# Optimization experiments

Hardware: AMD Instinct MI355X
Metric: run time of the kernel (lower is better)

Reference implementation:

```python
import jax, jax.numpy as jnp
import numpy as np

# --- MLA config (DeepSeek-V3 style, scaled) ---
HIDDEN = 4096
N_HEADS = 32
Q_LORA = 1536
KV_LORA = 512
ROPE_D = 64
NOPE_D = 128
V_D = 128
Q_HEAD_D = NOPE_D + ROPE_D  # 192
EPS = 1e-6
SCALING = Q_HEAD_D ** (-0.5)
ROPE_THETA = 10000.0
B, S = 1, 2048


def rms_norm(x, w):
    var = jnp.mean(jnp.square(x.astype(jnp.float32)), axis=-1, keepdims=True)
    return (x * jax.lax.rsqrt(var + EPS)).astype(x.dtype) * w


def rotate_half(x):
    x1, x2 = jnp.split(x, 2, axis=-1)
    return jnp.concatenate([-x2, x1], axis=-1)


def apply_rope(x, cos, sin):
    # x: [B, H, S, ROPE_D]; cos/sin: [B, S, ROPE_D] -> unsqueeze head dim
    c = cos[:, None, :, :]
    s = sin[:, None, :, :]
    return x * c + rotate_half(x) * s


def setup_inputs() -> dict:
    key = jax.random.key(0)
    ks = jax.random.split(key, 8)
    hidden_states = jax.random.normal(ks[0], (B, S, HIDDEN), dtype=jnp.float32)
    # real RoPE tables
    inv_freq = 1.0 / (ROPE_THETA ** (np.arange(0, ROPE_D, 2, dtype=np.float32) / ROPE_D))
    t = np.arange(S, dtype=np.float32)
    freqs = np.outer(t, inv_freq)                      # [S, ROPE_D/2]
    emb = np.concatenate([freqs, freqs], axis=-1)      # [S, ROPE_D]
    cos = jnp.asarray(np.cos(emb))[None].repeat(B, 0)  # [B, S, ROPE_D]
    sin = jnp.asarray(np.sin(emb))[None].repeat(B, 0)
    scale = lambda fan_in: 1.0 / np.sqrt(fan_in)
    w_q_a = jax.random.normal(ks[1], (Q_LORA, HIDDEN), dtype=jnp.float32) * scale(HIDDEN)
    q_a_ln_w = jnp.ones((Q_LORA,), dtype=jnp.float32)
    w_q_b = jax.random.normal(ks[2], (N_HEADS * Q_HEAD_D, Q_LORA), dtype=jnp.float32) * scale(Q_LORA)
    w_kv_a = jax.random.normal(ks[3], (KV_LORA + ROPE_D, HIDDEN), dtype=jnp.float32) * scale(HIDDEN)
    kv_a_ln_w = jnp.ones((KV_LORA,), dtype=jnp.float32)
    w_kv_b = jax.random.normal(ks[4], (N_HEADS * (NOPE_D + V_D), KV_LORA), dtype=jnp.float32) * scale(KV_LORA)
    w_o = jax.random.normal(ks[5], (HIDDEN, N_HEADS * V_D), dtype=jnp.float32) * scale(N_HEADS * V_D)
    return {
        'hidden_states': hidden_states, 'cos': cos, 'sin': sin,
        'w_q_a': w_q_a, 'q_a_ln_w': q_a_ln_w, 'w_q_b': w_q_b,
        'w_kv_a': w_kv_a, 'kv_a_ln_w': kv_a_ln_w, 'w_kv_b': w_kv_b, 'w_o': w_o,
    }


def reference(hidden_states, cos, sin, w_q_a, q_a_ln_w, w_q_b, w_kv_a, kv_a_ln_w, w_kv_b, w_o):
    b, s, _ = hidden_states.shape
    # --- Q path: low-rank down + RMSNorm + up ---
    q_lat = rms_norm(hidden_states @ w_q_a.T, q_a_ln_w)              # [B,S,Q_LORA]
    q = (q_lat @ w_q_b.T).reshape(b, s, N_HEADS, Q_HEAD_D)
    q = q.transpose(0, 2, 1, 3)                                       # [B,H,S,Q_HEAD_D]
    q_nope, q_rot = q[..., :NOPE_D], q[..., NOPE_D:]                  # (note: source names swapped)
    # --- KV path: shared compressed latent + single rotary key ---
    ckv = hidden_states @ w_kv_a.T                                    # [B,S,KV_LORA+ROPE_D]
    k_lat, k_rot = ckv[..., :KV_LORA], ckv[..., KV_LORA:]
    kv = (rms_norm(k_lat, kv_a_ln_w) @ w_kv_b.T).reshape(b, s, N_HEADS, NOPE_D + V_D)
    kv = kv.transpose(0, 2, 1, 3)                                     # [B,H,S,NOPE_D+V_D]
    k_nope, v = kv[..., :NOPE_D], kv[..., NOPE_D:]
    k_rot = k_rot.reshape(b, 1, s, ROPE_D)                            # single rotary key head
    # --- partial RoPE on rotary slices ---
    q_rot = apply_rope(q_rot, cos, sin)
    k_rot = apply_rope(k_rot, cos, sin)
    k_rot = jnp.broadcast_to(k_rot, (b, N_HEADS, s, ROPE_D))
    query = jnp.concatenate([q_rot, q_nope], axis=-1)                 # [B,H,S,192]
    key = jnp.concatenate([k_rot, k_nope], axis=-1)                   # [B,H,S,192]
    # --- eager causal attention ---
    scores = jnp.einsum('bhqd,bhkd->bhqk', query, key) * SCALING
    causal = jnp.tril(jnp.ones((s, s), dtype=bool))
    scores = jnp.where(causal[None, None], scores, jnp.finfo(scores.dtype).min)
    probs = jax.nn.softmax(scores, axis=-1)
    attn = jnp.einsum('bhqk,bhkd->bhqd', probs, v)                    # [B,H,S,V_D]
    attn = attn.transpose(0, 2, 1, 3).reshape(b, s, N_HEADS * V_D)
    return attn @ w_o.T                                               # [B,S,HIDDEN]
```

## Files before the change

kernel.cpp:

```cpp
#include <hip/hip_runtime.h>

typedef unsigned short u16;
typedef u16 u16x4 __attribute__((ext_vector_type(4)));
typedef u16 u16x8 __attribute__((ext_vector_type(8)));
typedef float f32x4 __attribute__((ext_vector_type(4)));
typedef __bf16 bf16x8 __attribute__((ext_vector_type(8)));

#define S_LEN 2048
#define HIDDEN_D 4096
#define NHEADS 32
#define QLORA 1536
#define KVLORA 512
#define ROPED 64
#define NOPED 128
#define VDIM 128
#define QHD 192
#define SCALING_F 0.07216878364870323f

__device__ __forceinline__ u16 f2bf(float x) {
  union { float f; unsigned u; } v; v.f = x;
  unsigned r = v.u + 0x7fffu + ((v.u >> 16) & 1u);
  return (u16)(r >> 16);
}
__device__ __forceinline__ float bf2f(u16 x) {
  union { unsigned u; float f; } v; v.u = ((unsigned)x) << 16; return v.f;
}

__device__ __forceinline__ f32x4 mfma_bf16(u16x8 a, u16x8 b, f32x4 c) {
  return __builtin_amdgcn_mfma_f32_16x16x32_bf16(
      __builtin_bit_cast(bf16x8, a), __builtin_bit_cast(bf16x8, b), c, 0, 0, 0);
}

__global__ __launch_bounds__(256) void cvt_kernel(const float* __restrict__ in,
                                                  u16* __restrict__ out, int n4) {
  int i = blockIdx.x * 256 + threadIdx.x;
  if (i >= n4) return;
  f32x4 v = ((const f32x4*)in)[i];
  u16x4 o;
  o[0] = f2bf(v[0]); o[1] = f2bf(v[1]); o[2] = f2bf(v[2]); o[3] = f2bf(v[3]);
  ((u16x4*)out)[i] = o;
}


#define GEMM_PROLOGUE()                                                        \
  __shared__ u16 sA[2][128 * 64];                                              \
  __shared__ u16 sB[2][128 * 64];                                              \
  const int tid = threadIdx.x;                                                 \
  const int wid = tid >> 6, lane = tid & 63;                                   \
  const int lr = lane & 15, lg = lane >> 4;                                    \
  const int nbn = (N + 127) >> 7;                                              \
  const int bx = blockIdx.x % nbn, by = blockIdx.x / nbn;                      \
  const int bm = by << 7, bn = bx << 7;                                        \
  const int wm = (wid >> 1) << 6, wn = (wid & 1) << 6;                         \
  const int kbase = blockIdx.y * Ks;                                           \
  f32x4 acc[4][4] = {};                                                        \
  u16x8 areg[4], breg[4];                                                      \
  auto loadA = [&](int k0) {                                                   \
    _Pragma("unroll")                                                          \
    for (int i = 0; i < 4; ++i) {                                              \
      int chunk = i * 256 + tid;                                               \
      int row = chunk >> 3, c8 = chunk & 7;                                    \
      int gr = bm + row; if (gr >= M) gr = M - 1;                              \
      areg[i] = *(const u16x8*)(A + (size_t)gr * lda + k0 + (c8 << 3));        \
    }                                                                          \
  };                                                                           \
  auto loadB = [&](int k0) {                                                   \
    _Pragma("unroll")                                                          \
    for (int i = 0; i < 4; ++i) {                                              \
      int chunk = i * 256 + tid;                                               \
      int n = chunk >> 3, c8 = chunk & 7;                                      \
      int gn = bn + n; if (gn >= N) gn = N - 1;                                \
      breg[i] = *(const u16x8*)(B + (size_t)gn * ldb + k0 + (c8 << 3));        \
    }                                                                          \
  };                                                                           \
  auto writeAB = [&](int buf) {                                                \
    _Pragma("unroll")                                                          \
    for (int i = 0; i < 4; ++i) {                                              \
      *(u16x8*)&sA[buf][(i * 256 + tid) * 8] = areg[i];                        \
      *(u16x8*)&sB[buf][(i * 256 + tid) * 8] = breg[i];                        \
    }                                                                          \
  };                                                                           \
  auto compute = [&](int buf) {                                                \
    const u16* pa = sA[buf];                                                   \
    const u16* pb = sB[buf];                                                   \
    _Pragma("unroll")                                                          \
    for (int ks = 0; ks < 2; ++ks) {                                           \
      const int kof = ks * 32 + lg * 8;                                        \
      u16x8 av[4], bv[4];                                                      \
      _Pragma("unroll")                                                        \
      for (int m = 0; m < 4; ++m) av[m] = *(const u16x8*)&pa[(wm + m * 16 + lr) * 64 + kof]; \
      _Pragma("unroll")                                                        \
      for (int n = 0; n < 4; ++n) bv[n] = *(const u16x8*)&pb[(wn + n * 16 + lr) * 64 + kof]; \
      _Pragma("unroll")                                                        \
      for (int m = 0; m < 4; ++m)                                              \
        _Pragma("unroll")                                                      \
        for (int n = 0; n < 4; ++n)                                            \
          acc[m][n] = mfma_bf16(av[m], bv[n], acc[m][n]);                      \
    }                                                                          \
  };                                                                           \
  const int nk = Ks >> 6;                                                      \
  loadA(kbase); loadB(kbase);                                                  \
  writeAB(0);                                                                  \
  __syncthreads();                                                             \
  for (int t = 0; t < nk; ++t) {                                               \
    const int cur = t & 1;                                                     \
    if (t + 1 < nk) { loadA(kbase + ((t + 1) << 6)); loadB(kbase + ((t + 1) << 6)); } \
    compute(cur);                                                              \
    if (t + 1 < nk) { writeAB(cur ^ 1); }                                      \
    __syncthreads();                                                           \
  }

__global__ __launch_bounds__(256, 2) void gemm_ff(
    const u16* __restrict__ A, const u16* __restrict__ B, float* __restrict__ C,
    int M, int N, int Ks, int lda, int ldb, int ldc)
{
  C += (size_t)blockIdx.y * M * ldc;
  GEMM_PROLOGUE()
#pragma unroll
  for (int m = 0; m < 4; ++m) {
    const int row0 = bm + wm + m * 16 + (lg << 2);
#pragma unroll
    for (int n = 0; n < 4; ++n) {
      const int col = bn + wn + n * 16 + lr;
      if (col < N) {
#pragma unroll
        for (int r = 0; r < 4; ++r)
          C[(size_t)(row0 + r) * ldc + col] = acc[m][n][r];
      }
    }
  }
}

__global__ __launch_bounds__(256, 2) void gemm_fb(
    const u16* __restrict__ A, const u16* __restrict__ B, u16* __restrict__ C,
    int M, int N, int Ks, int lda, int ldb, int ldc)
{
  GEMM_PROLOGUE()
#pragma unroll
  for (int m = 0; m < 4; ++m) {
    const int row0 = bm + wm + m * 16 + (lg << 2);
#pragma unroll
    for (int n = 0; n < 4; ++n) {
      const int col = bn + wn + n * 16 + lr;
#pragma unroll
      for (int r = 0; r < 4; ++r)
        C[(size_t)(row0 + r) * ldc + col] = f2bf(acc[m][n][r]);
    }
  }
}

__global__ __launch_bounds__(256, 2) void gemm_kvb(
    const u16* __restrict__ A, const u16* __restrict__ B,
    u16* __restrict__ Knope, u16* __restrict__ Vt,
    int M, int N, int Ks, int lda, int ldb)
{
  GEMM_PROLOGUE()
#pragma unroll
  for (int m = 0; m < 4; ++m) {
    const int row0 = bm + wm + m * 16 + (lg << 2);
#pragma unroll
    for (int n = 0; n < 4; ++n) {
      const int col = bn + wn + n * 16 + lr;
      const int h = col >> 8, c = col & 255;
      if (c < 128) {
#pragma unroll
        for (int r = 0; r < 4; ++r)
          Knope[((size_t)h * 2048 + row0 + r) * 128 + c] = f2bf(acc[m][n][r]);
      } else {
        u16x4 v;
        v[0] = f2bf(acc[m][n][0]); v[1] = f2bf(acc[m][n][1]);
        v[2] = f2bf(acc[m][n][2]); v[3] = f2bf(acc[m][n][3]);
        *(u16x4*)&Vt[((size_t)h * 128 + (c - 128)) * 2048 + row0] = v;
      }
    }
  }
}

__global__ __launch_bounds__(256) void rms_kernel(const float* __restrict__ X,
                                                  const float* __restrict__ w,
                                                  u16* __restrict__ out, int D, int ldx,
                                                  int nparts, size_t pstride) {
  const int row = blockIdx.x;
  const float* x = X + (size_t)row * ldx;
  __shared__ float sb[4];
  float ss = 0.f;
  for (int i = threadIdx.x * 4; i < D; i += 1024) {
    f32x4 v = *(const f32x4*)&x[i];
    for (int pp = 1; pp < nparts; ++pp) {
      f32x4 v2 = *(const f32x4*)&x[pp * pstride + i];
      v[0] += v2[0]; v[1] += v2[1]; v[2] += v2[2]; v[3] += v2[3];
    }
    ss += v[0] * v[0] + v[1] * v[1] + v[2] * v[2] + v[3] * v[3];
  }
#pragma unroll
  for (int off = 32; off >= 1; off >>= 1) ss += __shfl_xor(ss, off, 64);
  if ((threadIdx.x & 63) == 0) sb[threadIdx.x >> 6] = ss;
  __syncthreads();
  const float inv = rsqrtf((sb[0] + sb[1] + sb[2] + sb[3]) / (float)D + 1e-6f);
  u16* o = out + (size_t)row * D;
  for (int i = threadIdx.x * 4; i < D; i += 1024) {
    f32x4 v = *(const f32x4*)&x[i];
    for (int pp = 1; pp < nparts; ++pp) {
      f32x4 v2 = *(const f32x4*)&x[pp * pstride + i];
      v[0] += v2[0]; v[1] += v2[1]; v[2] += v2[2]; v[3] += v2[3];
    }
    f32x4 wv = *(const f32x4*)&w[i];
    u16x4 u;
    u[0] = f2bf(v[0] * inv * wv[0]); u[1] = f2bf(v[1] * inv * wv[1]);
    u[2] = f2bf(v[2] * inv * wv[2]); u[3] = f2bf(v[3] * inv * wv[3]);
    *(u16x4*)&o[i] = u;
  }
}

__global__ __launch_bounds__(256) void ckv_epi_kernel(const float* __restrict__ ckv,
    const float* __restrict__ w, const float* __restrict__ cosp, const float* __restrict__ sinp,
    u16* __restrict__ klatn, u16* __restrict__ krot, int ldx, int nparts, size_t pstride) {
  const int s = blockIdx.x;
  const float* x = ckv + (size_t)s * ldx;
  __shared__ float sb[4];
  const int i2 = threadIdx.x * 2;
  float a = 0.f, b = 0.f;
  for (int pp = 0; pp < nparts; ++pp) {
    a += x[pp * pstride + i2];
    b += x[pp * pstride + i2 + 1];
  }
  float ss = a * a + b * b;
#pragma unroll
  for (int off = 32; off >= 1; off >>= 1) ss += __shfl_xor(ss, off, 64);
  if ((threadIdx.x & 63) == 0) sb[threadIdx.x >> 6] = ss;
  __syncthreads();
  const float inv = rsqrtf((sb[0] + sb[1] + sb[2] + sb[3]) / 512.0f + 1e-6f);
  klatn[(size_t)s * 512 + i2]     = f2bf(a * inv * w[i2]);
  klatn[(size_t)s * 512 + i2 + 1] = f2bf(b * inv * w[i2 + 1]);
  if (threadIdx.x < 64) {
    const int d = threadIdx.x;
    float xr = 0.f, rrabs = 0.f;
    for (int pp = 0; pp < nparts; ++pp) {
      xr += x[pp * pstride + 512 + d];
      rrabs += x[pp * pstride + 512 + ((d < 32) ? (d + 32) : (d - 32))];
    }
    const float rr = (d < 32) ? -rrabs : rrabs;
    krot[(size_t)s * 64 + d] = f2bf(xr * cosp[s * 64 + d] + rr * sinp[s * 64 + d]);
  }
}

__global__ __launch_bounds__(256) void q_epi_kernel(const u16* __restrict__ q_raw,
    const float* __restrict__ cosp, const float* __restrict__ sinp, u16* __restrict__ Qb) {
  const int s = blockIdx.x;
  const u16* x = q_raw + (size_t)s * 6144;
  for (int idx = threadIdx.x; idx < 6144; idx += 256) {
    const int h = idx / 192, d = idx - h * 192;
    float v;
    if (d < 64) {
      const float xr = bf2f(x[h * 192 + 128 + d]);
      const float rr = (d < 32) ? -bf2f(x[h * 192 + 160 + d]) : bf2f(x[h * 192 + 96 + d]);
      v = xr * cosp[s * 64 + d] + rr * sinp[s * 64 + d];
    } else {
      v = bf2f(x[h * 192 + d - 64]);
    }
    Qb[((size_t)h * 2048 + s) * QHD + d] = f2bf(v * SCALING_F);
  }
}

__global__ __launch_bounds__(256, 2) void flash_kernel(
    const u16* __restrict__ Qb, const u16* __restrict__ Krot,
    const u16* __restrict__ Knope, const u16* __restrict__ Vt,
    u16* __restrict__ attnb)
{
  const int h = blockIdx.x & 31, qt = blockIdx.x >> 5;
  const int q0 = qt << 7;
  __shared__ u16 sK[64][QHD];
  __shared__ u16 sV[VDIM][64];
  __shared__ u16 sP[4][32][64];
  const int tid = threadIdx.x;
  const int wid = tid >> 6, lane = tid & 63;
  const int lr = lane & 15, lg = lane >> 4;

  u16x8 qf[2][6];
#pragma unroll
  for (int m = 0; m < 2; ++m) {
    const int row = q0 + wid * 32 + m * 16 + lr;
#pragma unroll
    for (int kk = 0; kk < 6; ++kk)
      qf[m][kk] = *(const u16x8*)&Qb[((size_t)h * 2048 + row) * QHD + kk * 32 + lg * 8];
  }

  f32x4 acc[2][8] = {};
  float mx[2][4], ls[2][4];
#pragma unroll
  for (int m = 0; m < 2; ++m)
#pragma unroll
    for (int r = 0; r < 4; ++r) { mx[m][r] = -1e30f; ls[m][r] = 0.f; }

  const int nkv = q0 + 128;
  u16x8 kreg[6], vreg[4];

  auto loadKV = [&](int kv0) {
#pragma unroll
    for (int i = 0; i < 6; ++i) {
      const int chunk = i * 256 + tid;
      const int row = chunk / 24, cc = chunk % 24;
      const u16* src = (cc < 8)
          ? &Krot[(size_t)(kv0 + row) * 64 + cc * 8]
          : &Knope[((size_t)h * 2048 + kv0 + row) * 128 + (cc - 8) * 8];
      kreg[i] = *(const u16x8*)src;
    }
#pragma unroll
    for (int i = 0; i < 4; ++i) {
      const int chunk = i * 256 + tid;
      const int d = chunk >> 3, c = chunk & 7;
      vreg[i] = *(const u16x8*)&Vt[((size_t)h * VDIM + d) * 2048 + kv0 + c * 8];
    }
  };

  loadKV(0);
  for (int kv0 = 0; kv0 < nkv; kv0 += 64) {
    __syncthreads();
    u16* kbase = &sK[0][0];
#pragma unroll
    for (int i = 0; i < 6; ++i) *(u16x8*)&kbase[(size_t)(i * 256 + tid) * 8] = kreg[i];
    u16* vbase = &sV[0][0];
#pragma unroll
    for (int i = 0; i < 4; ++i) *(u16x8*)&vbase[(size_t)(i * 256 + tid) * 8] = vreg[i];
    __syncthreads();
    if (kv0 + 64 < nkv) loadKV(kv0 + 64);

    f32x4 sc[2][4] = {};
#pragma unroll
    for (int kk = 0; kk < 6; ++kk) {
      u16x8 bfr[4];
#pragma unroll
      for (int n = 0; n < 4; ++n) bfr[n] = *(const u16x8*)&sK[n * 16 + lr][kk * 32 + lg * 8];
#pragma unroll
      for (int m = 0; m < 2; ++m)
#pragma unroll
        for (int n = 0; n < 4; ++n)
          sc[m][n] = mfma_bf16(qf[m][kk], bfr[n], sc[m][n]);
    }

    if (kv0 + 63 > q0 + wid * 32) {
#pragma unroll
      for (int m = 0; m < 2; ++m)
#pragma unroll
        for (int n = 0; n < 4; ++n) {
          const int kv = kv0 + n * 16 + lr;
#pragma unroll
          for (int r = 0; r < 4; ++r) {
            const int rowq = q0 + wid * 32 + m * 16 + lg * 4 + r;
            if (kv > rowq) sc[m][n][r] = -1e30f;
          }
        }
    }

#pragma unroll
    for (int m = 0; m < 2; ++m) {
      float rs[4];
#pragma unroll
      for (int r = 0; r < 4; ++r) {
        float v = fmaxf(fmaxf(sc[m][0][r], sc[m][1][r]), fmaxf(sc[m][2][r], sc[m][3][r]));
#pragma unroll
        for (int off = 1; off < 16; off <<= 1) v = fmaxf(v, __shfl_xor(v, off, 64));
        const float mnew = fmaxf(mx[m][r], v);
        const float alpha = __expf(mx[m][r] - mnew);
        mx[m][r] = mnew;
        ls[m][r] *= alpha;
#pragma unroll
        for (int df = 0; df < 8; ++df) acc[m][df][r] *= alpha;
        rs[r] = 0.f;
      }
#pragma unroll
      for (int n = 0; n < 4; ++n)
#pragma unroll
        for (int r = 0; r < 4; ++r) {
          const float p = __expf(sc[m][n][r] - mx[m][r]);
          rs[r] += p;
          sP[wid][m * 16 + lg * 4 + r][n * 16 + lr] = f2bf(p);
        }
#pragma unroll
      for (int r = 0; r < 4; ++r) {
        float v = rs[r];
#pragma unroll
        for (int off = 1; off < 16; off <<= 1) v += __shfl_xor(v, off, 64);
        ls[m][r] += v;
      }
    }

#pragma unroll
    for (int ks = 0; ks < 2; ++ks) {
      u16x8 pf0 = *(const u16x8*)&sP[wid][lr][ks * 32 + lg * 8];
      u16x8 pf1 = *(const u16x8*)&sP[wid][16 + lr][ks * 32 + lg * 8];
#pragma unroll
      for (int df = 0; df < 8; ++df) {
        u16x8 vf = *(const u16x8*)&sV[df * 16 + lr][ks * 32 + lg * 8];
        acc[0][df] = mfma_bf16(pf0, vf, acc[0][df]);
        acc[1][df] = mfma_bf16(pf1, vf, acc[1][df]);
      }
    }
  }

#pragma unroll
  for (int m = 0; m < 2; ++m)
#pragma unroll
    for (int df = 0; df < 8; ++df) {
      const int col = h * 128 + df * 16 + lr;
#pragma unroll
      for (int r = 0; r < 4; ++r) {
        const int row = q0 + wid * 32 + m * 16 + lg * 4 + r;
        attnb[(size_t)row * 4096 + col] = f2bf(acc[m][df][r] / ls[m][r]);
      }
    }
}

extern "C" void kernel_launch(void* const* d_in, const int* in_sizes, int n_in,
                              void* d_out, int out_size, void* d_ws, size_t ws_size,
                              hipStream_t stream) {
  (void)in_sizes; (void)n_in; (void)out_size; (void)ws_size;
  const float* hidden  = (const float*)d_in[0];
  const float* cosp    = (const float*)d_in[1];
  const float* sinp    = (const float*)d_in[2];
  const float* w_q_a   = (const float*)d_in[3];
  const float* q_a_ln  = (const float*)d_in[4];
  const float* w_q_b   = (const float*)d_in[5];
  const float* w_kv_a  = (const float*)d_in[6];
  const float* kv_a_ln = (const float*)d_in[7];
  const float* w_kv_b  = (const float*)d_in[8];
  const float* w_o     = (const float*)d_in[9];
  float* out = (float*)d_out;

  char* p = (char*)d_ws;
  auto alloc = [&](size_t bytes) { char* r = p; p += (bytes + 255) & ~(size_t)255; return r; };
  u16* Hb      = (u16*)alloc((size_t)S_LEN * HIDDEN_D * 2);
  u16* qlatn   = (u16*)alloc((size_t)S_LEN * QLORA * 2);
  u16* klatn   = (u16*)alloc((size_t)S_LEN * KVLORA * 2);
  u16* krot    = (u16*)alloc((size_t)S_LEN * ROPED * 2);
  u16* Qb      = (u16*)alloc((size_t)NHEADS * S_LEN * QHD * 2);
  u16* Knope   = (u16*)alloc((size_t)NHEADS * S_LEN * NOPED * 2);
  u16* Vt      = (u16*)alloc((size_t)NHEADS * VDIM * S_LEN * 2);
  u16* attnb   = (u16*)alloc((size_t)S_LEN * 4096 * 2);
  u16* WqaKva  = (u16*)alloc((size_t)2112 * HIDDEN_D * 2);
  u16* Wqb     = (u16*)alloc((size_t)6144 * QLORA * 2);
  u16* Wkvb    = (u16*)alloc((size_t)8192 * KVLORA * 2);
  u16* Wo      = (u16*)alloc((size_t)HIDDEN_D * 4096 * 2);
  u16* qraw16  = (u16*)alloc((size_t)S_LEN * 6144 * 2);
  float* qkv_part = (float*)alloc((size_t)2 * S_LEN * 2112 * 4);

  cvt_kernel<<<(S_LEN * HIDDEN_D / 4 + 255) / 256, 256, 0, stream>>>(hidden, Hb, S_LEN * HIDDEN_D / 4);
  cvt_kernel<<<(QLORA * HIDDEN_D / 4 + 255) / 256, 256, 0, stream>>>(w_q_a, WqaKva, QLORA * HIDDEN_D / 4);
  cvt_kernel<<<(576 * HIDDEN_D / 4 + 255) / 256, 256, 0, stream>>>(w_kv_a, WqaKva + (size_t)QLORA * HIDDEN_D, 576 * HIDDEN_D / 4);
  cvt_kernel<<<(6144 * QLORA / 4 + 255) / 256, 256, 0, stream>>>(w_q_b, Wqb, 6144 * QLORA / 4);
  cvt_kernel<<<(8192 * KVLORA / 4 + 255) / 256, 256, 0, stream>>>(w_kv_b, Wkvb, 8192 * KVLORA / 4);
  cvt_kernel<<<(HIDDEN_D * 4096 / 4 + 255) / 256, 256, 0, stream>>>(w_o, Wo, HIDDEN_D * 4096 / 4);

  gemm_ff<<<dim3(16 * 17, 2), 256, 0, stream>>>(Hb, WqaKva, qkv_part, 2048, 2112, 2048, 4096, 4096, 2112);
  rms_kernel<<<2048, 256, 0, stream>>>(qkv_part, q_a_ln, qlatn, 1536, 2112, 2, (size_t)S_LEN * 2112);
  ckv_epi_kernel<<<2048, 256, 0, stream>>>(qkv_part + 1536, kv_a_ln, cosp, sinp, klatn, krot, 2112, 2, (size_t)S_LEN * 2112);
  gemm_fb<<<dim3(16 * 48, 1), 256, 0, stream>>>(qlatn, Wqb, qraw16, 2048, 6144, 1536, 1536, 1536, 6144);
  q_epi_kernel<<<2048, 256, 0, stream>>>(qraw16, cosp, sinp, Qb);
  gemm_kvb<<<dim3(16 * 64, 1), 256, 0, stream>>>(klatn, Wkvb, Knope, Vt, 2048, 8192, 512, 512, 512);
  flash_kernel<<<512, 256, 0, stream>>>(Qb, krot, Knope, Vt, attnb);
  gemm_ff<<<dim3(16 * 32, 1), 256, 0, stream>>>(attnb, Wo, out, 2048, 4096, 4096, 4096, 4096, 4096);
}
```

Before: 598.9 us.

## Fuse q_b RoPE epilogue into GEMM, merge launches, permute Wqb rows

The five weight and activation conversion launches become one multi-range kernel. w_q_b is converted with a per-head row permutation so the rope columns come first. That lets the q_b GEMM apply RoPE and scaling in its epilogue and write Qb directly, removing the bf16 q_raw intermediate and the q_epi pass. The two RMS-norm kernels are merged into one launch, and the q_b and kv_b GEMMs now share a single grid. This trades fewer launches and less memory traffic for more scattered, uncoalesced epilogue stores and extra cos/sin loads per element.

```diff
diff --git a/kernel.cpp b/kernel.cpp
--- a/kernel.cpp
+++ b/kernel.cpp
@@ -31,25 +31,46 @@
       __builtin_bit_cast(bf16x8, a), __builtin_bit_cast(bf16x8, b), c, 0, 0, 0);
 }
 
-__global__ __launch_bounds__(256) void cvt_kernel(const float* __restrict__ in,
-                                                  u16* __restrict__ out, int n4) {
-  int i = blockIdx.x * 256 + threadIdx.x;
-  if (i >= n4) return;
-  f32x4 v = ((const f32x4*)in)[i];
+__global__ __launch_bounds__(256) void cvt_all(
+    const float* __restrict__ hsrc, u16* __restrict__ Hb,
+    const float* __restrict__ wqa, const float* __restrict__ wkva, u16* __restrict__ WqaKva,
+    const float* __restrict__ wkvb, u16* __restrict__ Wkvb,
+    const float* __restrict__ wo, u16* __restrict__ Wo)
+{
+  const int b = blockIdx.x, t = threadIdx.x;
+  const float* src; u16* dst; size_t idx;
+  if (b < 8192)       { src = hsrc; dst = Hb;     idx = (size_t)b * 256 + t; }
+  else if (b < 14336) { src = wqa;  dst = WqaKva; idx = (size_t)(b - 8192) * 256 + t; }
+  else if (b < 16640) { src = wkva; dst = WqaKva + (size_t)QLORA * HIDDEN_D; idx = (size_t)(b - 14336) * 256 + t; }
+  else if (b < 20736) { src = wkvb; dst = Wkvb;   idx = (size_t)(b - 16640) * 256 + t; }
+  else                { src = wo;   dst = Wo;     idx = (size_t)(b - 20736) * 256 + t; }
+  f32x4 v = ((const f32x4*)src)[idx];
   u16x4 o;
   o[0] = f2bf(v[0]); o[1] = f2bf(v[1]); o[2] = f2bf(v[2]); o[3] = f2bf(v[3]);
-  ((u16x4*)out)[i] = o;
-}
-
-
-#define GEMM_PROLOGUE()                                                        \
+  ((u16x4*)dst)[idx] = o;
+}
+
+__global__ __launch_bounds__(256) void cvt_qperm(const float* __restrict__ in,
+                                                 u16* __restrict__ out) {
+  const size_t idx = (size_t)blockIdx.x * 256 + threadIdx.x;
+  const int row = (int)(idx / 384), c4 = (int)(idx % 384);
+  const int h = row / 192, d = row - h * 192;
+  const int newd = (d >= 128) ? (d - 128) : (d + 64);
+  f32x4 v = ((const f32x4*)in)[idx];
+  u16x4 o;
+  o[0] = f2bf(v[0]); o[1] = f2bf(v[1]); o[2] = f2bf(v[2]); o[3] = f2bf(v[3]);
+  ((u16x4*)out)[(size_t)(h * 192 + newd) * 384 + c4] = o;
+}
+
+
+#define GEMM_PROLOGUE(BIDX)                                                    \
   __shared__ u16 sA[2][128 * 64];                                              \
   __shared__ u16 sB[2][128 * 64];                                              \
   const int tid = threadIdx.x;                                                 \
   const int wid = tid >> 6, lane = tid & 63;                                   \
   const int lr = lane & 15, lg = lane >> 4;                                    \
   const int nbn = (N + 127) >> 7;                                              \
-  const int bx = blockIdx.x % nbn, by = blockIdx.x / nbn;                      \
+  const int bx = (BIDX) % nbn, by = (BIDX) / nbn;                              \
   const int bm = by << 7, bn = bx << 7;                                        \
   const int wm = (wid >> 1) << 6, wn = (wid & 1) << 6;                         \
   const int kbase = blockIdx.y * Ks;                                           \
@@ -115,7 +136,7 @@
     int M, int N, int Ks, int lda, int ldb, int ldc)
 {
   C += (size_t)blockIdx.y * M * ldc;
-  GEMM_PROLOGUE()
+  GEMM_PROLOGUE(blockIdx.x)
 #pragma unroll
   for (int m = 0; m < 4; ++m) {
     const int row0 = bm + wm + m * 16 + (lg << 2);
@@ -131,134 +152,130 @@
   }
 }
 
-__global__ __launch_bounds__(256, 2) void gemm_fb(
-    const u16* __restrict__ A, const u16* __restrict__ B, u16* __restrict__ C,
-    int M, int N, int Ks, int lda, int ldb, int ldc)
+__global__ __launch_bounds__(256, 2) void gemm_qb_kvb(
+    const u16* __restrict__ qlatn, const u16* __restrict__ Wqb,
+    const float* __restrict__ cosp, const float* __restrict__ sinp, u16* __restrict__ Qb,
+    const u16* __restrict__ klatn, const u16* __restrict__ Wkvb,
+    u16* __restrict__ Knope, u16* __restrict__ Vt)
 {
-  GEMM_PROLOGUE()
-#pragma unroll
-  for (int m = 0; m < 4; ++m) {
-    const int row0 = bm + wm + m * 16 + (lg << 2);
-#pragma unroll
-    for (int n = 0; n < 4; ++n) {
-      const int col = bn + wn + n * 16 + lr;
-#pragma unroll
-      for (int r = 0; r < 4; ++r)
-        C[(size_t)(row0 + r) * ldc + col] = f2bf(acc[m][n][r]);
-    }
-  }
-}
-
-__global__ __launch_bounds__(256, 2) void gemm_kvb(
-    const u16* __restrict__ A, const u16* __restrict__ B,
-    u16* __restrict__ Knope, u16* __restrict__ Vt,
-    int M, int N, int Ks, int lda, int ldb)
+  if (blockIdx.x < 768) {
+    const u16* A = qlatn; const u16* B = Wqb;
+    const int M = 2048, N = 6144, Ks = 1536, lda = 1536, ldb = 1536;
+    GEMM_PROLOGUE(blockIdx.x)
+#pragma unroll
+    for (int m = 0; m < 4; ++m) {
+      const int row0 = bm + wm + m * 16 + (lg << 2);
+#pragma unroll
+      for (int n = 0; n < 2; ++n) {
+        const int col = bn + wn + n * 16 + lr;
+        const int h = col / 192, tc = col - h * 192;
+        if (tc < 32) {
+#pragma unroll
+          for (int r = 0; r < 4; ++r) {
+            const int s = row0 + r;
+            const float cx = cosp[s * 64 + tc],      sx = sinp[s * 64 + tc];
+            const float cy = cosp[s * 64 + tc + 32], sy = sinp[s * 64 + tc + 32];
+            const float xv = acc[m][n][r], yv = acc[m][n + 2][r];
+            Qb[((size_t)h * 2048 + s) * QHD + tc]      = f2bf((xv * cx - yv * sx) * SCALING_F);
+            Qb[((size_t)h * 2048 + s) * QHD + tc + 32] = f2bf((yv * cy + xv * sy) * SCALING_F);
+          }
+        }
+      }
+#pragma unroll
+      for (int n = 0; n < 4; ++n) {
+        const int col = bn + wn + n * 16 + lr;
+        const int h = col / 192, tc = col - h * 192;
+        if (tc >= 64) {
+#pragma unroll
+          for (int r = 0; r < 4; ++r) {
+            const int s = row0 + r;
+            Qb[((size_t)h * 2048 + s) * QHD + tc] = f2bf(acc[m][n][r] * SCALING_F);
+          }
+        }
+      }
+    }
+  } else {
+    const u16* A = klatn; const u16* B = Wkvb;
+    const int M = 2048, N = 8192, Ks = 512, lda = 512, ldb = 512;
+    GEMM_PROLOGUE(blockIdx.x - 768)
+#pragma unroll
+    for (int m = 0; m < 4; ++m) {
+      const int row0 = bm + wm + m * 16 + (lg << 2);
+#pragma unroll
+      for (int n = 0; n < 4; ++n) {
+        const int col = bn + wn + n * 16 + lr;
+        const int h = col >> 8, c = col & 255;
+        if (c < 128) {
+#pragma unroll
+          for (int r = 0; r < 4; ++r)
+            Knope[((size_t)h * 2048 + row0 + r) * 128 + c] = f2bf(acc[m][n][r]);
+        } else {
+          u16x4 v;
+          v[0] = f2bf(acc[m][n][0]); v[1] = f2bf(acc[m][n][1]);
+          v[2] = f2bf(acc[m][n][2]); v[3] = f2bf(acc[m][n][3]);
+          *(u16x4*)&Vt[((size_t)h * 128 + (c - 128)) * 2048 + row0] = v;
+        }
+      }
+    }
+  }
+}
+
+__global__ __launch_bounds__(256) void norm_fused(
+    const float* __restrict__ qkv_part,
+    const float* __restrict__ q_a_ln, const float* __restrict__ kv_a_ln,
+    const float* __restrict__ cosp, const float* __restrict__ sinp,
+    u16* __restrict__ qlatn, u16* __restrict__ klatn, u16* __restrict__ krot)
 {
-  GEMM_PROLOGUE()
-#pragma unroll
-  for (int m = 0; m < 4; ++m) {
-    const int row0 = bm + wm + m * 16 + (lg << 2);
-#pragma unroll
-    for (int n = 0; n < 4; ++n) {
-      const int col = bn + wn + n * 16 + lr;
-      const int h = col >> 8, c = col & 255;
-      if (c < 128) {
-#pragma unroll
-        for (int r = 0; r < 4; ++r)
-          Knope[((size_t)h * 2048 + row0 + r) * 128 + c] = f2bf(acc[m][n][r]);
-      } else {
-        u16x4 v;
-        v[0] = f2bf(acc[m][n][0]); v[1] = f2bf(acc[m][n][1]);
-        v[2] = f2bf(acc[m][n][2]); v[3] = f2bf(acc[m][n][3]);
-        *(u16x4*)&Vt[((size_t)h * 128 + (c - 128)) * 2048 + row0] = v;
-      }
-    }
-  }
-}
-
-__global__ __launch_bounds__(256) void rms_kernel(const float* __restrict__ X,
-                                                  const float* __restrict__ w,
-                                                  u16* __restrict__ out, int D, int ldx,
-                                                  int nparts, size_t pstride) {
-  const int row = blockIdx.x;
-  const float* x = X + (size_t)row * ldx;
+  const size_t PSTRIDE = (size_t)S_LEN * 2112;
   __shared__ float sb[4];
-  float ss = 0.f;
-  for (int i = threadIdx.x * 4; i < D; i += 1024) {
-    f32x4 v = *(const f32x4*)&x[i];
-    for (int pp = 1; pp < nparts; ++pp) {
-      f32x4 v2 = *(const f32x4*)&x[pp * pstride + i];
+  if (blockIdx.x < 2048) {
+    const int row = blockIdx.x;
+    const float* x = qkv_part + (size_t)row * 2112;
+    float ss = 0.f;
+    for (int i = threadIdx.x * 4; i < 1536; i += 1024) {
+      f32x4 v = *(const f32x4*)&x[i];
+      f32x4 v2 = *(const f32x4*)&x[PSTRIDE + i];
       v[0] += v2[0]; v[1] += v2[1]; v[2] += v2[2]; v[3] += v2[3];
-    }
-    ss += v[0] * v[0] + v[1] * v[1] + v[2] * v[2] + v[3] * v[3];
-  }
-#pragma unroll
-  for (int off = 32; off >= 1; off >>= 1) ss += __shfl_xor(ss, off, 64);
-  if ((threadIdx.x & 63) == 0) sb[threadIdx.x >> 6] = ss;
-  __syncthreads();
-  const float inv = rsqrtf((sb[0] + sb[1] + sb[2] + sb[3]) / (float)D + 1e-6f);
-  u16* o = out + (size_t)row * D;
-  for (int i = threadIdx.x * 4; i < D; i += 1024) {
-    f32x4 v = *(const f32x4*)&x[i];
-    for (int pp = 1; pp < nparts; ++pp) {
-      f32x4 v2 = *(const f32x4*)&x[pp * pstride + i];
+      ss += v[0] * v[0] + v[1] * v[1] + v[2] * v[2] + v[3] * v[3];
+    }
+#pragma unroll
+    for (int off = 32; off >= 1; off >>= 1) ss += __shfl_xor(ss, off, 64);
+    if ((threadIdx.x & 63) == 0) sb[threadIdx.x >> 6] = ss;
+    __syncthreads();
+    const float inv = rsqrtf((sb[0] + sb[1] + sb[2] + sb[3]) / 1536.0f + 1e-6f);
+    u16* o = qlatn + (size_t)row * 1536;
+    for (int i = threadIdx.x * 4; i < 1536; i += 1024) {
+      f32x4 v = *(const f32x4*)&x[i];
+      f32x4 v2 = *(const f32x4*)&x[PSTRIDE + i];
       v[0] += v2[0]; v[1] += v2[1]; v[2] += v2[2]; v[3] += v2[3];
-    }
-    f32x4 wv = *(const f32x4*)&w[i];
-    u16x4 u;
-    u[0] = f2bf(v[0] * inv * wv[0]); u[1] = f2bf(v[1] * inv * wv[1]);
-    u[2] = f2bf(v[2] * inv * wv[2]); u[3] = f2bf(v[3] * inv * wv[3]);
-    *(u16x4*)&o[i] = u;
-  }
-}
-
-__global__ __launch_bounds__(256) void ckv_epi_kernel(const float* __restrict__ ckv,
-    const float* __restrict__ w, const float* __restrict__ cosp, const float* __restrict__ sinp,
-    u16* __restrict__ klatn, u16* __restrict__ krot, int ldx, int nparts, size_t pstride) {
-  const int s = blockIdx.x;
-  const float* x = ckv + (size_t)s * ldx;
-  __shared__ float sb[4];
-  const int i2 = threadIdx.x * 2;
-  float a = 0.f, b = 0.f;
-  for (int pp = 0; pp < nparts; ++pp) {
-    a += x[pp * pstride + i2];
-    b += x[pp * pstride + i2 + 1];
-  }
-  float ss = a * a + b * b;
-#pragma unroll
-  for (int off = 32; off >= 1; off >>= 1) ss += __shfl_xor(ss, off, 64);
-  if ((threadIdx.x & 63) == 0) sb[threadIdx.x >> 6] = ss;
-  __syncthreads();
-  const float inv = rsqrtf((sb[0] + sb[1] + sb[2] + sb[3]) / 512.0f + 1e-6f);
-  klatn[(size_t)s * 512 + i2]     = f2bf(a * inv * w[i2]);
-  klatn[(size_t)s * 512 + i2 + 1] = f2bf(b * inv * w[i2 + 1]);
-  if (threadIdx.x < 64) {
-    const int d = threadIdx.x;
-    float xr = 0.f, rrabs = 0.f;
-    for (int pp = 0; pp < nparts; ++pp) {
-      xr += x[pp * pstride + 512 + d];
-      rrabs += x[pp * pstride + 512 + ((d < 32) ? (d + 32) : (d - 32))];
-    }
-    const float rr = (d < 32) ? -rrabs : rrabs;
-    krot[(size_t)s * 64 + d] = f2bf(xr * cosp[s * 64 + d] + rr * sinp[s * 64 + d]);
-  }
-}
-
-__global__ __launch_bounds__(256) void q_epi_kernel(const u16* __restrict__ q_raw,
-    const float* __restrict__ cosp, const float* __restrict__ sinp, u16* __restrict__ Qb) {
-  const int s = blockIdx.x;
-  const u16* x = q_raw + (size_t)s * 6144;
-  for (int idx = threadIdx.x; idx < 6144; idx += 256) {
-    const int h = idx / 192, d = idx - h * 192;
-    float v;
-    if (d < 64) {
-      const float xr = bf2f(x[h * 192 + 128 + d]);
-      const float rr = (d < 32) ? -bf2f(x[h * 192 + 160 + d]) : bf2f(x[h * 192 + 96 + d]);
-      v = xr * cosp[s * 64 + d] + rr * sinp[s * 64 + d];
-    } else {
-      v = bf2f(x[h * 192 + d - 64]);
-    }
-    Qb[((size_t)h * 2048 + s) * QHD + d] = f2bf(v * SCALING_F);
+      f32x4 wv = *(const f32x4*)&q_a_ln[i];
+      u16x4 u;
+      u[0] = f2bf(v[0] * inv * wv[0]); u[1] = f2bf(v[1] * inv * wv[1]);
+      u[2] = f2bf(v[2] * inv * wv[2]); u[3] = f2bf(v[3] * inv * wv[3]);
+      *(u16x4*)&o[i] = u;
+    }
+  } else {
+    const int s = blockIdx.x - 2048;
+    const float* x = qkv_part + 1536 + (size_t)s * 2112;
+    const int i2 = threadIdx.x * 2;
+    float a = x[i2] + x[PSTRIDE + i2];
+    float b = x[i2 + 1] + x[PSTRIDE + i2 + 1];
+    float ss = a * a + b * b;
+#pragma unroll
+    for (int off = 32; off >= 1; off >>= 1) ss += __shfl_xor(ss, off, 64);
+    if ((threadIdx.x & 63) == 0) sb[threadIdx.x >> 6] = ss;
+    __syncthreads();
+    const float inv = rsqrtf((sb[0] + sb[1] + sb[2] + sb[3]) / 512.0f + 1e-6f);
+    klatn[(size_t)s * 512 + i2]     = f2bf(a * inv * kv_a_ln[i2]);
+    klatn[(size_t)s * 512 + i2 + 1] = f2bf(b * inv * kv_a_ln[i2 + 1]);
+    if (threadIdx.x < 64) {
+      const int d = threadIdx.x;
+      const float xr = x[512 + d] + x[PSTRIDE + 512 + d];
+      const int dp = (d < 32) ? (d + 32) : (d - 32);
+      const float rrabs = x[512 + dp] + x[PSTRIDE + 512 + dp];
+      const float rr = (d < 32) ? -rrabs : rrabs;
+      krot[(size_t)s * 64 + d] = f2bf(xr * cosp[s * 64 + d] + rr * sinp[s * 64 + d]);
+    }
   }
 }
 
@@ -441,22 +458,13 @@
   u16* Wqb     = (u16*)alloc((size_t)6144 * QLORA * 2);
   u16* Wkvb    = (u16*)alloc((size_t)8192 * KVLORA * 2);
   u16* Wo      = (u16*)alloc((size_t)HIDDEN_D * 4096 * 2);
-  u16* qraw16  = (u16*)alloc((size_t)S_LEN * 6144 * 2);
   float* qkv_part = (float*)alloc((size_t)2 * S_LEN * 2112 * 4);
 
-  cvt_kernel<<<(S_LEN * HIDDEN_D / 4 + 255) / 256, 256, 0, stream>>>(hidden, Hb, S_LEN * HIDDEN_D / 4);
-  cvt_kernel<<<(QLORA * HIDDEN_D / 4 + 255) / 256, 256, 0, stream>>>(w_q_a, WqaKva, QLORA * HIDDEN_D / 4);
-  cvt_kernel<<<(576 * HIDDEN_D / 4 + 255) / 256, 256, 0, stream>>>(w_kv_a, WqaKva + (size_t)QLORA * HIDDEN_D, 576 * HIDDEN_D / 4);
-  cvt_kernel<<<(6144 * QLORA / 4 + 255) / 256, 256, 0, stream>>>(w_q_b, Wqb, 6144 * QLORA / 4);
-  cvt_kernel<<<(8192 * KVLORA / 4 + 255) / 256, 256, 0, stream>>>(w_kv_b, Wkvb, 8192 * KVLORA / 4);
-  cvt_kernel<<<(HIDDEN_D * 4096 / 4 + 255) / 256, 256, 0, stream>>>(w_o, Wo, HIDDEN_D * 4096 / 4);
-
+  cvt_all<<<37120, 256, 0, stream>>>(hidden, Hb, w_q_a, w_kv_a, WqaKva, w_kv_b, Wkvb, w_o, Wo);
+  cvt_qperm<<<9216, 256, 0, stream>>>(w_q_b, Wqb);
   gemm_ff<<<dim3(16 * 17, 2), 256, 0, stream>>>(Hb, WqaKva, qkv_part, 2048, 2112, 2048, 4096, 4096, 2112);
-  rms_kernel<<<2048, 256, 0, stream>>>(qkv_part, q_a_ln, qlatn, 1536, 2112, 2, (size_t)S_LEN * 2112);
-  ckv_epi_kernel<<<2048, 256, 0, stream>>>(qkv_part + 1536, kv_a_ln, cosp, sinp, klatn, krot, 2112, 2, (size_t)S_LEN * 2112);
-  gemm_fb<<<dim3(16 * 48, 1), 256, 0, stream>>>(qlatn, Wqb, qraw16, 2048, 6144, 1536, 1536, 1536, 6144);
-  q_epi_kernel<<<2048, 256, 0, stream>>>(qraw16, cosp, sinp, Qb);
-  gemm_kvb<<<dim3(16 * 64, 1), 256, 0, stream>>>(klatn, Wkvb, Knope, Vt, 2048, 8192, 512, 512, 512);
+  norm_fused<<<4096, 256, 0, stream>>>(qkv_part, q_a_ln, kv_a_ln, cosp, sinp, qlatn, klatn, krot);
+  gemm_qb_kvb<<<768 + 1024, 256, 0, stream>>>(qlatn, Wqb, cosp, sinp, Qb, klatn, Wkvb, Knope, Vt);
   flash_kernel<<<512, 256, 0, stream>>>(Qb, krot, Knope, Vt, attnb);
   gemm_ff<<<dim3(16 * 32, 1), 256, 0, stream>>>(attnb, Wo, out, 2048, 4096, 4096, 4096, 4096, 4096);
 }
```

Measured after the change: 608.9 us. About the same (+1.7%).
